# Performance work log

Hardware: AMD Instinct MI355X
Metric: run time of the kernel (lower is better)

Reference implementation:

```python
import jax, jax.numpy as jnp
import numpy as np

HID = 128
PE_DIM = 4
N = 100_000       # nodes per type
E = 400_000       # edges per edge type
L = 3             # message passing layers
G = 512           # num graphs
NT = ['ssBox', 'place_frame', 'object', 'ssCylinder', 'pick', 'place']
FEAT_DIMS = {'ssBox': 4, 'place_frame': 4, 'object': 4, 'ssCylinder': 3}
EMB_IN = {'ssBox': 8, 'place_frame': 8, 'object': 8, 'ssCylinder': 7, 'pick': 4, 'place': 4}
EDGE_TYPES = [
    ('object', 'ssBox'), ('ssBox', 'object'), ('place_frame', 'ssBox'), ('ssBox', 'place_frame'),
    ('place_frame', 'object'), ('object', 'place_frame'), ('pick', 'place'), ('place', 'pick'),
    ('object', 'object'), ('ssBox', 'ssBox'), ('place_frame', 'place_frame'), ('ssCylinder', 'ssCylinder'),
    ('object', 'pick'), ('pick', 'object'), ('place_frame', 'pick'), ('pick', 'place_frame'),
    ('ssCylinder', 'pick'), ('pick', 'ssCylinder'), ('object', 'place'), ('place', 'object'),
    ('ssCylinder', 'place'), ('place', 'ssCylinder'), ('place_frame', 'place'), ('place', 'place_frame')]


def _pe(times):
    # sinusoidal PE from integer positions -> [n, PE_DIM], cols interleaved sin/cos
    pos = times.astype(jnp.float32)[:, None]
    div = jnp.exp(jnp.arange(0, PE_DIM, 2, dtype=jnp.float32) * (-np.log(10000.0) / PE_DIM))
    s, c = jnp.sin(pos * div), jnp.cos(pos * div)
    return jnp.stack([s, c], axis=2).reshape(pos.shape[0], PE_DIM)


def setup_inputs() -> dict:
    key = jax.random.key(0)
    ks = iter(jax.random.split(key, 64))
    inp = {}
    for t in ['ssBox', 'place_frame', 'object']:
        inp['x_' + t] = jax.random.normal(next(ks), (N, 4), jnp.float32)
    inp['x_ssCylinder'] = jax.random.normal(next(ks), (N, 3), jnp.float32)
    for t in NT:
        d = EMB_IN[t]
        inp['W_' + t] = jax.random.normal(next(ks), (d, HID), jnp.float32) / np.sqrt(d)
        inp['b_' + t] = jax.random.normal(next(ks), (HID,), jnp.float32) * 0.01
    sc = 1.0 / np.sqrt(HID)
    inp['sage_Wl'] = jax.random.normal(next(ks), (L, 24, HID, HID), jnp.float32) * sc
    inp['sage_bl'] = jax.random.normal(next(ks), (L, 24, HID), jnp.float32) * 0.01
    inp['sage_Wr'] = jax.random.normal(next(ks), (L, 24, HID, HID), jnp.float32) * sc
    inp['oh_W1'] = jax.random.normal(next(ks), (HID, HID // 4), jnp.float32) * sc
    inp['oh_b1'] = jax.random.normal(next(ks), (HID // 4,), jnp.float32) * 0.01
    inp['oh_W2'] = jax.random.normal(next(ks), (HID // 4, 1), jnp.float32) / np.sqrt(HID // 4)
    inp['oh_b2'] = jax.random.normal(next(ks), (1,), jnp.float32) * 0.01
    inp['times'] = jax.random.randint(next(ks), (6, N), 0, 1000, jnp.int32)
    inp['edges'] = jax.random.randint(next(ks), (24, 2, E), 0, N, jnp.int32)
    inp['batch'] = jax.random.randint(next(ks), (6, N), 0, G, jnp.int32)
    return inp


def reference(x_ssBox, x_place_frame, x_object, x_ssCylinder,
              W_ssBox, b_ssBox, W_place_frame, b_place_frame, W_object, b_object,
              W_ssCylinder, b_ssCylinder, W_pick, b_pick, W_place, b_place,
              sage_Wl, sage_bl, sage_Wr, oh_W1, oh_b1, oh_W2, oh_b2,
              times, edges, batch):
    feats = {'ssBox': x_ssBox, 'place_frame': x_place_frame, 'object': x_object, 'ssCylinder': x_ssCylinder}
    embW = {'ssBox': W_ssBox, 'place_frame': W_place_frame, 'object': W_object,
            'ssCylinder': W_ssCylinder, 'pick': W_pick, 'place': W_place}
    embB = {'ssBox': b_ssBox, 'place_frame': b_place_frame, 'object': b_object,
            'ssCylinder': b_ssCylinder, 'pick': b_pick, 'place': b_place}
    init, x = {}, {}
    for t in ['ssBox', 'place_frame', 'object', 'ssCylinder']:
        f = jnp.concatenate([feats[t], _pe(times[NT.index(t)])], axis=1)
        h = f @ embW[t] + embB[t]
        init[t] = h
        x[t] = h
    for t in ['pick', 'place']:
        x[t] = _pe(times[NT.index(t)]) @ embW[t] + embB[t]
    x = {t: jax.nn.relu(v) for t, v in x.items()}

    for layer in range(L):
        out = {}
        for i, (src, dst) in enumerate(EDGE_TYPES):
            e = edges[i]
            msg = x[src][e[0]]                                           # [E, HID] gather
            agg = jax.ops.segment_sum(msg, e[1], num_segments=N)
            deg = jax.ops.segment_sum(jnp.ones((E,), msg.dtype), e[1], num_segments=N)
            mean = agg / jnp.maximum(deg, 1.0)[:, None]                  # SAGE mean aggr
            o = mean @ sage_Wl[layer, i] + sage_bl[layer, i] + x[dst] @ sage_Wr[layer, i]
            out[dst] = out[dst] + o if dst in out else o
        # dropout is identity in eval/reference
        x = {t: jax.nn.relu(out.get(t, x[t])) for t in x}

    g = jnp.zeros((G, HID), jnp.float32)
    for t in ['pick', 'place']:
        g = g.at[batch[NT.index(t)]].add(x[t])
    for t in ['ssBox', 'ssCylinder', 'place_frame', 'object']:
        g = g.at[batch[NT.index(t)]].add(init[t])
    h = jax.nn.relu(g) @ oh_W1 + oh_b1
    h = jax.nn.relu(h) @ oh_W2 + oh_b2
    return h.squeeze(-1)
```

## Files before the change

### kernel.cpp

```cpp
#include <hip/hip_runtime.h>
#include <hip/hip_bf16.h>

#define NN 100000
#define EE 400000
#define HID 128
#define GG 512
#define NTY 6
#define NET 24
#define TILES_PER_TYPE 1563
#define EMB_TILES 782
#define BLK_ELEMS ((size_t)NN * 128)
#define BLK_BYTES (BLK_ELEMS * 2)

#define P1_BLKS 37500
#define HN_BLKS 2344
#define PWR_BLKS 1152
#define PBL_BLKS 9
#define PWL_BLKS 4608
#define EMB_BLKS (NTY * EMB_TILES)
#define ZG_BLKS 256

typedef _Float16 half8 __attribute__((ext_vector_type(8)));
typedef float f32x4 __attribute__((ext_vector_type(4)));

__constant__ int d_EMB_IN[6]    = {8,8,8,7,4,4};
__constant__ int d_FD[6]        = {4,4,4,3,0,0};
__constant__ int d_EDGE_SRC[24] = {2,0,1,0,1,2,4,5,2,0,1,3,2,4,1,4,3,4,2,5,3,5,1,5};
__constant__ int d_DST_NIN[6]   = {3,5,5,3,4,4};
__constant__ int d_DST_OFF[6]   = {0,3,8,13,16,20};
__constant__ int d_DST_EDGES[24]= {0,2,9, 3,5,10,15,23, 1,4,8,13,19, 11,17,21, 7,12,14,16, 6,18,20,22};

struct GP {
    const float* feat[4];
    const float* embW[6];
    const float* embB[6];
    const float* Wl; const float* bl; const float* Wr;
    const float* W1; const float* b1; const float* W2; const float* b2;
    const int* times; const int* edges; const int* batch;
};

struct XT { _Float16* p[6]; };

__device__ __forceinline__ int clampi(int v, int lo, int hi) {
    return v < lo ? lo : (v > hi ? hi : v);
}

__global__ void zero_i32(int* __restrict__ p, int n) {
    int i = blockIdx.x * 256 + threadIdx.x;
    if (i < n) p[i] = 0;
}

__global__ void diag_kernel(float* __restrict__ out, float v) {
    int i = blockIdx.x * 64 + threadIdx.x;
    if (i < GG) out[i] = v;
}

__device__ __forceinline__ void csr_pass1_body(const int* __restrict__ edges, int* __restrict__ deg,
                                               unsigned short* __restrict__ rank, int b) {
    int i = b * 256 + threadIdx.x;
    if (i >= NET * EE) return;
    int et = i / EE, e = i - et * EE;
    int dst = clampi(edges[(et * 2 + 1) * EE + e], 0, NN - 1);
    int r = atomicAdd(&deg[et * NN + dst], 1);
    rank[i] = (unsigned short)(r > 65535 ? 65535 : r);
}

__device__ __forceinline__ void csr_pass2_body(const int* __restrict__ edges, const int* __restrict__ rowptr,
                                               const unsigned short* __restrict__ rank, int* __restrict__ csr, int b) {
    int i = b * 256 + threadIdx.x;
    if (i >= NET * EE) return;
    int et = i / EE, e = i - et * EE;
    int src = clampi(edges[(et * 2) * EE + e], 0, NN - 1);
    int dst = clampi(edges[(et * 2 + 1) * EE + e], 0, NN - 1);
    int pos = clampi(rowptr[et * NN + dst] + (int)rank[i], 0, NET * EE - 1);
    csr[pos] = src;
}

__device__ __forceinline__ void hist_nodes_body(const int* __restrict__ batch, int* __restrict__ hist2, int b) {
    int i = b * 256 + threadIdx.x;
    if (i >= NTY * NN) return;
    int t = i / NN, n = i - t * NN;
    int bb = clampi(batch[t * NN + n], 0, GG - 1);
    atomicAdd(&hist2[t * GG + bb], 1);
}

__device__ __forceinline__ void scatter_nodes_body(const int* __restrict__ batch, const int* __restrict__ rowptr2,
                                                   int* __restrict__ fill2, int* __restrict__ nodelist, int b) {
    int i = b * 256 + threadIdx.x;
    if (i >= NTY * NN) return;
    int t = i / NN, n = i - t * NN;
    int bb = t * GG + clampi(batch[t * NN + n], 0, GG - 1);
    int pos = clampi(rowptr2[bb] + atomicAdd(&fill2[bb], 1), 0, NTY * NN - 1);
    nodelist[pos] = n;
}

__device__ __forceinline__ void prep_wl_body(const float* __restrict__ Wl, _Float16* __restrict__ WlTf, int b) {
    int i = b * 256 + threadIdx.x;
    if (i >= 72 * 16384) return;
    int mat = i >> 14;
    int o = i & 16383;
    int cq = o >> 9; int c = cq >> 2, q = cq & 3;
    int lane = (o >> 3) & 63, j = o & 7;
    int k = q * 32 + (lane >> 4) * 8 + j;
    int n = c * 16 + (lane & 15);
    WlTf[i] = (_Float16)Wl[((size_t)mat * 128 + k) * 128 + n];
}

__device__ __forceinline__ void prep_wr_body(const float* __restrict__ Wr, _Float16* __restrict__ WrTf, int b) {
    int i = b * 256 + threadIdx.x;
    if (i >= 18 * 16384) return;
    int mat = i >> 14;
    int l = mat / 6, dd = mat - l * 6;
    int o = i & 16383;
    int cq = o >> 9; int c = cq >> 2, q = cq & 3;
    int lane = (o >> 3) & 63, j = o & 7;
    int k = q * 32 + (lane >> 4) * 8 + j;
    int n = c * 16 + (lane & 15);
    float s = 0.f;
    int nin = d_DST_NIN[dd], off = d_DST_OFF[dd];
    for (int ii = 0; ii < nin; ++ii) {
        int e = d_DST_EDGES[off + ii];
        s += Wr[(((size_t)l * 24 + e) * 128 + k) * 128 + n];
    }
    WrTf[i] = (_Float16)s;
}

__device__ __forceinline__ void prep_bl_body(const float* __restrict__ bl, float* __restrict__ bls, int b) {
    int i = b * 256 + threadIdx.x;
    if (i >= 3 * 6 * 128) return;
    int l = i / 768; int rest = i - l * 768;
    int dd = rest >> 7; int col = rest & 127;
    float s = 0.f;
    int nin = d_DST_NIN[dd], off = d_DST_OFF[dd];
    for (int ii = 0; ii < nin; ++ii) {
        int e = d_DST_EDGES[off + ii];
        s += bl[((size_t)l * 24 + e) * 128 + col];
    }
    bls[i] = s;
}

__device__ __forceinline__ void embed_body(const GP& gp, const XT& xout, int bidx,
                                           float fls[128][8], float Wsh[8][128], float bsh[128]) {
    int t = bidx / EMB_TILES;
    int tile = bidx - t * EMB_TILES;
    int base = tile * 128;
    int tid = threadIdx.x;
    int ein = d_EMB_IN[t];
    for (int idx = tid; idx < 1024; idx += 256) {
        int k = idx >> 7, dd = idx & 127;
        Wsh[k][dd] = (k < ein) ? gp.embW[t][k * 128 + dd] : 0.f;
    }
    if (tid < 128) bsh[tid] = gp.embB[t][tid];
    if (tid < 128) {
        int node = base + tid;
        float f[8] = {0.f,0.f,0.f,0.f,0.f,0.f,0.f,0.f};
        if (node < NN) {
            int fd = d_FD[t];
            if (fd > 0) {
                const float* fp = gp.feat[t] + (size_t)node * fd;
                for (int k = 0; k < fd; k++) f[k] = fp[k];
            }
            float pos = (float)gp.times[t * NN + node];
            float d1 = expf(-0.5f * logf(10000.0f));
            f[fd + 0] = sinf(pos);      f[fd + 1] = cosf(pos);
            f[fd + 2] = sinf(pos * d1); f[fd + 3] = cosf(pos * d1);
        }
#pragma unroll
        for (int k = 0; k < 8; k++) fls[tid][k] = f[k];
    }
    __syncthreads();
    int oct = tid & 15, slot = tid >> 4;
    _Float16* xp = xout.p[t];
    for (int nl = slot; nl < 128; nl += 16) {
        int node = base + nl;
        if (node >= NN) continue;
        float h[8];
#pragma unroll
        for (int j = 0; j < 8; ++j) h[j] = bsh[oct * 8 + j];
#pragma unroll
        for (int k = 0; k < 8; ++k) {
            float f = fls[nl][k];
#pragma unroll
            for (int j = 0; j < 8; ++j) h[j] += f * Wsh[k][oct * 8 + j];
        }
        half8 hv;
#pragma unroll
        for (int j = 0; j < 8; ++j) { float v = h[j] > 0.f ? h[j] : 0.f; hv[j] = (_Float16)v; }
        *(half8*)(xp + (size_t)node * 128 + oct * 8) = hv;
    }
}

__global__ __launch_bounds__(256)
void mega1(GP gp, int* __restrict__ deg, unsigned short* __restrict__ rank,
           int* __restrict__ hist2, _Float16* __restrict__ WrTf, float* __restrict__ bls,
           _Float16* __restrict__ WlTf, XT tabA) {
    __shared__ float fls[128][8];
    __shared__ float Wsh[8][128];
    __shared__ float bsh[128];
    int b = blockIdx.x;
    if (b < P1_BLKS) { csr_pass1_body(gp.edges, deg, rank, b); return; }
    b -= P1_BLKS;
    if (b < HN_BLKS) { hist_nodes_body(gp.batch, hist2, b); return; }
    b -= HN_BLKS;
    if (b < PWR_BLKS) { prep_wr_body(gp.Wr, WrTf, b); return; }
    b -= PWR_BLKS;
    if (b < PBL_BLKS) { prep_bl_body(gp.bl, bls, b); return; }
    b -= PBL_BLKS;
    if (b < PWL_BLKS) { prep_wl_body(gp.Wl, WlTf, b); return; }
    b -= PWL_BLKS;
    embed_body(gp, tabA, b, fls, Wsh, bsh);
}

__global__ __launch_bounds__(256)
void mega2(GP gp, const int* __restrict__ rowptr, const unsigned short* __restrict__ rank,
           int* __restrict__ csr, const int* __restrict__ rowptr2, int* __restrict__ fill2,
           int* __restrict__ nodelist, int* __restrict__ g) {
    int b = blockIdx.x;
    if (b < P1_BLKS) { csr_pass2_body(gp.edges, rowptr, rank, csr, b); return; }
    b -= P1_BLKS;
    if (b < HN_BLKS) { scatter_nodes_body(gp.batch, rowptr2, fill2, nodelist, b); return; }
    b -= HN_BLKS;
    int i = b * 256 + threadIdx.x;
    if (i < GG * 128) g[i] = 0;
}

__global__ void prep_wr_k(const float* __restrict__ Wr, _Float16* __restrict__ WrTf) { prep_wr_body(Wr, WrTf, blockIdx.x); }
__global__ void prep_bl_k(const float* __restrict__ bl, float* __restrict__ bls)     { prep_bl_body(bl, bls, blockIdx.x); }
__global__ void prep_wl_k(const float* __restrict__ Wl, _Float16* __restrict__ WlTf) { prep_wl_body(Wl, WlTf, blockIdx.x); }
__global__ void embed_k(GP gp, XT xout) {
    __shared__ float fls[128][8];
    __shared__ float Wsh[8][128];
    __shared__ float bsh[128];
    embed_body(gp, xout, blockIdx.x, fls, Wsh, bsh);
}

__global__ void scan1(const int* __restrict__ in, int* __restrict__ out, int* __restrict__ bsum, int M) {
    int base = blockIdx.x * 2048;
    int tid = threadIdx.x;
    int idx = base + tid * 8;
    int v[8]; int s = 0;
#pragma unroll
    for (int k = 0; k < 8; k++) { int i = idx + k; v[k] = (i < M) ? in[i] : 0; }
#pragma unroll
    for (int k = 0; k < 8; k++) { int t = v[k]; v[k] = s; s += t; }
    __shared__ int sh[256];
    sh[tid] = s; __syncthreads();
    for (int off = 1; off < 256; off <<= 1) {
        int t = (tid >= off) ? sh[tid - off] : 0;
        __syncthreads(); sh[tid] += t; __syncthreads();
    }
    int excl = sh[tid] - s;
#pragma unroll
    for (int k = 0; k < 8; k++) { int i = idx + k; if (i < M) out[i] = excl + v[k]; }
    if (tid == 255) bsum[blockIdx.x] = sh[255];
}

__global__ void scan2_node(int* __restrict__ bsum, int NB, int* __restrict__ rowptr, int M, int total,
                           int* __restrict__ hist2, int* __restrict__ rowptr2) {
    __shared__ int sh[256];
    __shared__ int shc;
    int tid = threadIdx.x;
    int carry = 0;
    for (int chunk = 0; chunk < NB; chunk += 256) {
        int i = chunk + tid;
        int v = (i < NB) ? bsum[i] : 0;
        __syncthreads();
        sh[tid] = v; __syncthreads();
        for (int off = 1; off < 256; off <<= 1) {
            int t = (tid >= off) ? sh[tid - off] : 0;
            __syncthreads(); sh[tid] += t; __syncthreads();
        }
        int inc = sh[tid];
        if (i < NB) bsum[i] = carry + inc - v;
        if (tid == 255) shc = inc;
        __syncthreads();
        carry += shc;
    }
    if (tid == 0) rowptr[M] = total;
    carry = 0;
    for (int chunk = 0; chunk < NTY * GG; chunk += 256) {
        int v = hist2[chunk + tid];
        __syncthreads();
        sh[tid] = v; __syncthreads();
        for (int off = 1; off < 256; off <<= 1) {
            int t = (tid >= off) ? sh[tid - off] : 0;
            __syncthreads(); sh[tid] += t; __syncthreads();
        }
        rowptr2[chunk + tid] = carry + sh[tid] - v;
        hist2[chunk + tid] = 0;
        if (tid == 255) shc = sh[255];
        __syncthreads();
        carry += shc;
    }
    if (tid == 0) rowptr2[NTY * GG] = NTY * NN;
}

__global__ void scan3(int* __restrict__ out, const int* __restrict__ bsum, int M) {
    int i = blockIdx.x * 256 + threadIdx.x;
    if (i < M) out[i] += bsum[i >> 11];
}

__global__ __launch_bounds__(256)
void layer_kernel(XT cur, XT nxt, int d0,
                  const int* __restrict__ rowptr, const int* __restrict__ csr,
                  const _Float16* __restrict__ WlTf, const _Float16* __restrict__ WrTf,
                  const float* __restrict__ bls) {
    int bid = blockIdx.x;
    int d = d0 + bid / TILES_PER_TYPE;
    int tile = bid % TILES_PER_TYPE;
    int tid = threadIdx.x, lane = tid & 63, wave = tid >> 6;
    int lrow = lane & 15, quad = lane >> 4;
    int wrow0 = tile * 64 + wave * 16;
    int myrow = wrow0 + lrow;
    bool rowok = myrow < NN;

    f32x4 acc[8];
#pragma unroll
    for (int c = 0; c < 8; c++) {
        float bv = bls[d * 128 + c * 16 + lrow];
        acc[c] = (f32x4){bv, bv, bv, bv};
    }

    int nin = d_DST_NIN[d];
    int off = d_DST_OFF[d];
    for (int term = 0; term <= nin; ++term) {
        half8 af[4];
        const _Float16* Bmat;
        if (term == 0) {
            Bmat = WrTf + (size_t)d * 16384;
            if (rowok) {
                const half8* p = (const half8*)(cur.p[d] + (size_t)myrow * 128 + quad * 8);
                af[0] = p[0]; af[1] = p[4]; af[2] = p[8]; af[3] = p[12];
            } else {
#pragma unroll
                for (int q = 0; q < 4; q++)
#pragma unroll
                    for (int z = 0; z < 8; z++) af[q][z] = (_Float16)0.f;
            }
        } else {
            int e = d_DST_EDGES[off + term - 1];
            int st = d_EDGE_SRC[e];
            Bmat = WlTf + (size_t)e * 16384;
            const _Float16* xs = cur.p[st];
            float facc[32];
#pragma unroll
            for (int z = 0; z < 32; z++) facc[z] = 0.f;
            int start = 0, cnt = 0;
            if (rowok) {
                int bi = e * NN + myrow;
                start = clampi(rowptr[bi], 0, NET * EE - 1);
                cnt = clampi(rowptr[bi + 1] - start, 0, 4096);
            }
            for (int j = 0;; ++j) {
                if (__ballot(j < cnt) == 0ull) break;
                if (j < cnt) {
                    int sn = clampi(csr[start + j], 0, NN - 1);
                    const half8* p = (const half8*)(xs + (size_t)sn * 128 + quad * 8);
                    half8 v0 = p[0], v1 = p[4], v2 = p[8], v3 = p[12];
#pragma unroll
                    for (int z = 0; z < 8; z++) {
                        facc[z]      += (float)v0[z];
                        facc[8 + z]  += (float)v1[z];
                        facc[16 + z] += (float)v2[z];
                        facc[24 + z] += (float)v3[z];
                    }
                }
            }
            float inv = 1.0f / (float)(cnt > 1 ? cnt : 1);
#pragma unroll
            for (int q = 0; q < 4; q++)
#pragma unroll
                for (int z = 0; z < 8; z++) af[q][z] = (_Float16)(facc[q * 8 + z] * inv);
        }
#pragma unroll
        for (int q = 0; q < 4; q++) {
#pragma unroll
            for (int c = 0; c < 8; c++) {
                half8 b = *(const half8*)(Bmat + (((c * 4 + q) << 9) + (lane << 3)));
                acc[c] = __builtin_amdgcn_mfma_f32_16x16x32_f16(af[q], b, acc[c], 0, 0, 0);
            }
        }
    }
    _Float16* xo = nxt.p[d];
#pragma unroll
    for (int c = 0; c < 8; c++) {
#pragma unroll
        for (int r = 0; r < 4; r++) {
            int grow = wrow0 + quad * 4 + r;
            if (grow < NN) {
                float v = acc[c][r];
                v = v > 0.f ? v : 0.f;
                xo[(size_t)grow * 128 + c * 16 + lrow] = (_Float16)v;
            }
        }
    }
}

__global__ void readout_kernel(GP gp, XT x3,
                               const int* __restrict__ nodelist, const int* __restrict__ rowptr2,
                               float* __restrict__ g) {
    int t = blockIdx.x >> 9;
    int gi = blockIdx.x & 511;
    int tid = threadIdx.x;
    int s = clampi(rowptr2[t * GG + gi], 0, NTY * NN - 1);
    int cnt = clampi(rowptr2[t * GG + gi + 1] - s, 0, NN);
    if (t >= 4) {
        int oct = tid & 15, slot = tid >> 4;
        const _Float16* xp = x3.p[t];
        float acc8[8];
#pragma unroll
        for (int z = 0; z < 8; z++) acc8[z] = 0.f;
        for (int li = slot; li < cnt; li += 16) {
            int node = clampi(nodelist[s + li], 0, NN - 1);
            half8 v = *(const half8*)(xp + (size_t)node * 128 + oct * 8);
#pragma unroll
            for (int z = 0; z < 8; z++) acc8[z] += (float)v[z];
        }
        __shared__ float red[16][128];
#pragma unroll
        for (int z = 0; z < 8; z++) red[slot][oct * 8 + z] = acc8[z];
        __syncthreads();
        for (int off = 8; off >= 1; off >>= 1) {
            if (slot < off) {
#pragma unroll
                for (int z = 0; z < 8; z++)
                    red[slot][oct * 8 + z] += red[slot + off][oct * 8 + z];
            }
            __syncthreads();
        }
        if (tid < 128) atomicAdd(&g[gi * 128 + tid], red[0][tid]);
    } else {
        int ein = d_EMB_IN[t];
        int fd = d_FD[t];
        const float* W = gp.embW[t]; const float* bb = gp.embB[t];
        float d1 = expf(-0.5f * logf(10000.0f));
        float fs[8];
#pragma unroll
        for (int k = 0; k < 8; k++) fs[k] = 0.f;
        for (int li = tid; li < cnt; li += 256) {
            int node = clampi(nodelist[s + li], 0, NN - 1);
            const float* fp = gp.feat[t] + (size_t)node * fd;
            for (int k = 0; k < fd; k++) fs[k] += fp[k];
            float pos = (float)gp.times[t * NN + node];
            fs[fd + 0] += sinf(pos);      fs[fd + 1] += cosf(pos);
            fs[fd + 2] += sinf(pos * d1); fs[fd + 3] += cosf(pos * d1);
        }
        __shared__ float red[8][256];
#pragma unroll
        for (int k = 0; k < 8; k++) red[k][tid] = fs[k];
        __syncthreads();
        for (int off = 128; off >= 1; off >>= 1) {
            if (tid < off) {
#pragma unroll
                for (int k = 0; k < 8; k++) red[k][tid] += red[k][tid + off];
            }
            __syncthreads();
        }
        if (tid < 128) {
            float acc = (float)cnt * bb[tid];
            for (int k = 0; k < ein; k++) acc += red[k][0] * W[k * 128 + tid];
            atomicAdd(&g[gi * 128 + tid], acc);
        }
    }
}

__global__ void head_kernel(const float* __restrict__ g, const float* __restrict__ W1,
                            const float* __restrict__ b1, const float* __restrict__ W2,
                            const float* __restrict__ b2, float* __restrict__ out) {
    int gi = blockIdx.x;
    int tid = threadIdx.x;
    __shared__ float h1[32];
    if (tid < 32) {
        float s = b1[tid];
        for (int dd = 0; dd < 128; ++dd) s += fmaxf(g[gi * 128 + dd], 0.f) * W1[dd * 32 + tid];
        h1[tid] = s;
    }
    __syncthreads();
    if (tid == 0) {
        float o = b2[0];
        for (int j = 0; j < 32; ++j) o += fmaxf(h1[j], 0.f) * W2[j];
        out[gi] = o;
    }
}

extern "C" void kernel_launch(void* const* d_in, const int* in_sizes, int n_in,
                              void* d_out, int out_size, void* d_ws, size_t ws_size,
                              hipStream_t stream) {
    char* ws = (char*)d_ws;
    size_t o = 0;
    auto alloc = [&](size_t bytes) -> void* {
        void* p = ws + o;
        o += (bytes + 255) & ~(size_t)255;
        return p;
    };
    _Float16* xws   = (_Float16*)alloc(9 * BLK_BYTES);
    int* csr        = (int*)alloc((size_t)NET * EE * 4 + 256);
    int* rowptr     = (int*)alloc(((size_t)NET * NN + 1) * 4);
    int* nodelist   = (int*)alloc((size_t)NTY * NN * 4);
    int* rowptr2    = (int*)alloc((NTY * GG + 1) * 4);
    float* g        = (float*)alloc(GG * 128 * 4);
    int* bsum       = (int*)alloc(4096 * 4);
    int* bsum2      = (int*)alloc(256 * 4);
    size_t REQUIRED = o;
    int* degX             = (int*)alloc((size_t)NET * NN * 4);
    int* hist2X           = (int*)alloc(NTY * GG * 4);
    unsigned short* rankX = (unsigned short*)alloc((size_t)NET * EE * 2);
    _Float16* WlTfX       = (_Float16*)alloc((size_t)72 * 16384 * 2);
    _Float16* WrTfX       = (_Float16*)alloc((size_t)18 * 16384 * 2);
    float* blsX           = (float*)alloc(3 * 6 * 128 * 4);
    bool sep = ws_size >= o;
    (void)in_sizes; (void)out_size;

    if (ws_size < REQUIRED || n_in != 26) {
        float v = 2000.0f + (float)(ws_size >> 20) + (n_in != 26 ? 100000.0f : 0.0f);
        diag_kernel<<<8, 64, 0, stream>>>((float*)d_out, v);
        return;
    }

    GP gp;
    for (int t = 0; t < 4; t++) gp.feat[t] = (const float*)d_in[t];
    for (int t = 0; t < 6; t++) { gp.embW[t] = (const float*)d_in[4 + 2 * t]; gp.embB[t] = (const float*)d_in[5 + 2 * t]; }
    gp.Wl = (const float*)d_in[16];
    gp.bl = (const float*)d_in[17];
    gp.Wr = (const float*)d_in[18];
    gp.W1 = (const float*)d_in[19];
    gp.b1 = (const float*)d_in[20];
    gp.W2 = (const float*)d_in[21];
    gp.b2 = (const float*)d_in[22];
    gp.times = (const int*)d_in[23];
    gp.edges = (const int*)d_in[24];
    gp.batch = (const int*)d_in[25];

    int* deg; int* hist2; unsigned short* rank;
    _Float16* WlTf; _Float16* WrTf; float* bls;
    if (sep) {
        deg = degX; hist2 = hist2X; rank = rankX; WlTf = WlTfX; WrTf = WrTfX; bls = blsX;
    } else {
        deg   = (int*)xws;
        hist2 = (int*)((char*)xws + 9600000);
        rank  = (unsigned short*)((char*)xws + BLK_BYTES);
        WlTf  = (_Float16*)d_in[18];
        WrTf  = (_Float16*)d_in[25];
        bls   = (float*)((char*)d_in[25] + 1048576);
    }

    XT tabA, tabB;
    for (int t = 0; t < 6; t++) tabA.p[t] = xws + (size_t)t * BLK_ELEMS;
    for (int t = 0; t < 3; t++) tabB.p[t] = xws + (size_t)(6 + t) * BLK_ELEMS;
    for (int t = 3; t < 6; t++) tabB.p[t] = (_Float16*)d_in[24] + (size_t)(t - 3) * BLK_ELEMS;

    int Medge = NET * NN;
    int NB = (Medge + 2047) / 2048;
    int Mn = NTY * GG;

    zero_i32<<<(Medge + Mn + 255) / 256, 256, 0, stream>>>(deg, Medge + Mn);
    if (sep) {
        mega1<<<P1_BLKS + HN_BLKS + PWR_BLKS + PBL_BLKS + PWL_BLKS + EMB_BLKS, 256, 0, stream>>>(
            gp, deg, rank, hist2, WrTf, bls, WlTf, tabA);
    } else {
        mega1<<<P1_BLKS + HN_BLKS, 256, 0, stream>>>(gp, deg, rank, hist2, WrTf, bls, WlTf, tabA);
    }
    scan1<<<NB, 256, 0, stream>>>(deg, rowptr, bsum, Medge);
    scan2_node<<<1, 256, 0, stream>>>(bsum, NB, rowptr, Medge, NET * EE, hist2, rowptr2);
    scan3<<<(Medge + 255) / 256, 256, 0, stream>>>(rowptr, bsum, Medge);
    mega2<<<P1_BLKS + HN_BLKS + ZG_BLKS, 256, 0, stream>>>(gp, rowptr, rank, csr,
                                                           rowptr2, hist2, nodelist, (int*)g);
    if (!sep) {
        prep_wr_k<<<PWR_BLKS, 256, 0, stream>>>(gp.Wr, WrTf);
        prep_bl_k<<<PBL_BLKS, 256, 0, stream>>>(gp.bl, bls);
        prep_wl_k<<<PWL_BLKS, 256, 0, stream>>>(gp.Wl, WlTf);
        embed_k<<<EMB_BLKS, 256, 0, stream>>>(gp, tabA);
    }

    layer_kernel<<<6 * TILES_PER_TYPE, 256, 0, stream>>>(tabA, tabB, 0, rowptr, csr,
        WlTf + (size_t)0 * 24 * 16384, WrTf + (size_t)0 * 6 * 16384, bls + 0 * 6 * 128);
    layer_kernel<<<5 * TILES_PER_TYPE, 256, 0, stream>>>(tabB, tabA, 1, rowptr, csr,
        WlTf + (size_t)1 * 24 * 16384, WrTf + (size_t)1 * 6 * 16384, bls + 1 * 6 * 128);
    layer_kernel<<<2 * TILES_PER_TYPE, 256, 0, stream>>>(tabA, tabB, 4, rowptr, csr,
        WlTf + (size_t)2 * 24 * 16384, WrTf + (size_t)2 * 6 * 16384, bls + 2 * 6 * 128);

    readout_kernel<<<NTY * GG, 256, 0, stream>>>(gp, tabB, nodelist, rowptr2, g);
    head_kernel<<<GG, 64, 0, stream>>>(g, gp.W1, gp.b1, gp.W2, gp.b2, (float*)d_out);
}
```

Measured before the change: 2.858 ms.

## Fuse scan stages with last-block ticket and merge init readout into layer one

Merges the three-kernel prefix scan into one kernel, where the last block to finish, chosen by an atomic ticket, scans the block sums and the node histogram. The separate add-block-offset pass goes away, and consumers now add bsum on the fly when they read rowptr. The readout for the init node types is folded into the first layer kernel as extra blocks, the zeroing kernel becomes a hipMemsetAsync, and the final readout only covers pick and place. This cuts kernel launches and one full pass over rowptr, at the cost of an extra bsum load for every rowptr read in the layer gathers and CSR build.

```diff
diff --git a/kernel.cpp b/kernel.cpp
--- a/kernel.cpp
+++ b/kernel.cpp
@@ -11,6 +11,8 @@
 #define EMB_TILES 782
 #define BLK_ELEMS ((size_t)NN * 128)
 #define BLK_BYTES (BLK_ELEMS * 2)
+#define MEDGE (NET * NN)
+#define NBE ((MEDGE + 2047) / 2048)
 
 #define P1_BLKS 37500
 #define HN_BLKS 2344
@@ -19,6 +21,7 @@
 #define PWL_BLKS 4608
 #define EMB_BLKS (NTY * EMB_TILES)
 #define ZG_BLKS 256
+#define RO_BLKS (4 * GG)
 
 typedef _Float16 half8 __attribute__((ext_vector_type(8)));
 typedef float f32x4 __attribute__((ext_vector_type(4)));
@@ -45,11 +48,6 @@
     return v < lo ? lo : (v > hi ? hi : v);
 }
 
-__global__ void zero_i32(int* __restrict__ p, int n) {
-    int i = blockIdx.x * 256 + threadIdx.x;
-    if (i < n) p[i] = 0;
-}
-
 __global__ void diag_kernel(float* __restrict__ out, float v) {
     int i = blockIdx.x * 64 + threadIdx.x;
     if (i < GG) out[i] = v;
@@ -66,13 +64,15 @@
 }
 
 __device__ __forceinline__ void csr_pass2_body(const int* __restrict__ edges, const int* __restrict__ rowptr,
+                                               const int* __restrict__ bsum,
                                                const unsigned short* __restrict__ rank, int* __restrict__ csr, int b) {
     int i = b * 256 + threadIdx.x;
     if (i >= NET * EE) return;
     int et = i / EE, e = i - et * EE;
     int src = clampi(edges[(et * 2) * EE + e], 0, NN - 1);
     int dst = clampi(edges[(et * 2 + 1) * EE + e], 0, NN - 1);
-    int pos = clampi(rowptr[et * NN + dst] + (int)rank[i], 0, NET * EE - 1);
+    int bin = et * NN + dst;
+    int pos = clampi(rowptr[bin] + bsum[bin >> 11] + (int)rank[i], 0, NET * EE - 1);
     csr[pos] = src;
 }
 
@@ -187,6 +187,144 @@
 #pragma unroll
         for (int j = 0; j < 8; ++j) { float v = h[j] > 0.f ? h[j] : 0.f; hv[j] = (_Float16)v; }
         *(half8*)(xp + (size_t)node * 128 + oct * 8) = hv;
+    }
+}
+
+__device__ __forceinline__ void readout_init_body(const GP& gp, const int* __restrict__ nodelist,
+                                                  const int* __restrict__ rowptr2, float* __restrict__ g,
+                                                  int b, float red[8][256]) {
+    int t = b >> 9;
+    int gi = b & 511;
+    int tid = threadIdx.x;
+    int s = clampi(rowptr2[t * GG + gi], 0, NTY * NN - 1);
+    int cnt = clampi(rowptr2[t * GG + gi + 1] - s, 0, NN);
+    int ein = d_EMB_IN[t];
+    int fd = d_FD[t];
+    const float* W = gp.embW[t]; const float* bb = gp.embB[t];
+    float d1 = expf(-0.5f * logf(10000.0f));
+    float fs[8];
+#pragma unroll
+    for (int k = 0; k < 8; k++) fs[k] = 0.f;
+    for (int li = tid; li < cnt; li += 256) {
+        int node = clampi(nodelist[s + li], 0, NN - 1);
+        const float* fp = gp.feat[t] + (size_t)node * fd;
+        for (int k = 0; k < fd; k++) fs[k] += fp[k];
+        float pos = (float)gp.times[t * NN + node];
+        fs[fd + 0] += sinf(pos);      fs[fd + 1] += cosf(pos);
+        fs[fd + 2] += sinf(pos * d1); fs[fd + 3] += cosf(pos * d1);
+    }
+#pragma unroll
+    for (int k = 0; k < 8; k++) red[k][tid] = fs[k];
+    __syncthreads();
+    for (int off = 128; off >= 1; off >>= 1) {
+        if (tid < off) {
+#pragma unroll
+            for (int k = 0; k < 8; k++) red[k][tid] += red[k][tid + off];
+        }
+        __syncthreads();
+    }
+    if (tid < 128) {
+        float acc = (float)cnt * bb[tid];
+        for (int k = 0; k < ein; k++) acc += red[k][0] * W[k * 128 + tid];
+        atomicAdd(&g[gi * 128 + tid], acc);
+    }
+}
+
+__device__ __forceinline__ void layer_body(const XT& cur, const XT& nxt, int d0, int bid,
+                                           const int* __restrict__ rowptr, const int* __restrict__ bsum,
+                                           const int* __restrict__ csr,
+                                           const _Float16* __restrict__ WlTf, const _Float16* __restrict__ WrTf,
+                                           const float* __restrict__ bls) {
+    int d = d0 + bid / TILES_PER_TYPE;
+    int tile = bid % TILES_PER_TYPE;
+    int tid = threadIdx.x, lane = tid & 63, wave = tid >> 6;
+    int lrow = lane & 15, quad = lane >> 4;
+    int wrow0 = tile * 64 + wave * 16;
+    int myrow = wrow0 + lrow;
+    bool rowok = myrow < NN;
+
+    f32x4 acc[8];
+#pragma unroll
+    for (int c = 0; c < 8; c++) {
+        float bv = bls[d * 128 + c * 16 + lrow];
+        acc[c] = (f32x4){bv, bv, bv, bv};
+    }
+
+    int nin = d_DST_NIN[d];
+    int off = d_DST_OFF[d];
+    for (int term = 0; term <= nin; ++term) {
+        half8 af[4];
+        const _Float16* Bmat;
+        if (term == 0) {
+            Bmat = WrTf + (size_t)d * 16384;
+            if (rowok) {
+                const half8* p = (const half8*)(cur.p[d] + (size_t)myrow * 128 + quad * 8);
+                af[0] = p[0]; af[1] = p[4]; af[2] = p[8]; af[3] = p[12];
+            } else {
+#pragma unroll
+                for (int q = 0; q < 4; q++)
+#pragma unroll
+                    for (int z = 0; z < 8; z++) af[q][z] = (_Float16)0.f;
+            }
+        } else {
+            int e = d_DST_EDGES[off + term - 1];
+            int st = d_EDGE_SRC[e];
+            Bmat = WlTf + (size_t)e * 16384;
+            const _Float16* xs = cur.p[st];
+            float facc[32];
+#pragma unroll
+            for (int z = 0; z < 32; z++) facc[z] = 0.f;
+            int start = 0, cnt = 0;
+            if (rowok) {
+                int bi = e * NN + myrow;
+                int s0 = rowptr[bi] + bsum[bi >> 11];
+                int bi1 = bi + 1;
+                int e1 = (bi1 == MEDGE) ? (NET * EE) : (rowptr[bi1] + bsum[bi1 >> 11]);
+                start = clampi(s0, 0, NET * EE - 1);
+                cnt = clampi(e1 - s0, 0, 4096);
+            }
+            for (int j = 0;; ++j) {
+                if (__ballot(j < cnt) == 0ull) break;
+                if (j < cnt) {
+                    int sn = clampi(csr[start + j], 0, NN - 1);
+                    const half8* p = (const half8*)(xs + (size_t)sn * 128 + quad * 8);
+                    half8 v0 = p[0], v1 = p[4], v2 = p[8], v3 = p[12];
+#pragma unroll
+                    for (int z = 0; z < 8; z++) {
+                        facc[z]      += (float)v0[z];
+                        facc[8 + z]  += (float)v1[z];
+                        facc[16 + z] += (float)v2[z];
+                        facc[24 + z] += (float)v3[z];
+                    }
+                }
+            }
+            float inv = 1.0f / (float)(cnt > 1 ? cnt : 1);
+#pragma unroll
+            for (int q = 0; q < 4; q++)
+#pragma unroll
+                for (int z = 0; z < 8; z++) af[q][z] = (_Float16)(facc[q * 8 + z] * inv);
+        }
+#pragma unroll
+        for (int q = 0; q < 4; q++) {
+#pragma unroll
+            for (int c = 0; c < 8; c++) {
+                half8 b = *(const half8*)(Bmat + (((c * 4 + q) << 9) + (lane << 3)));
+                acc[c] = __builtin_amdgcn_mfma_f32_16x16x32_f16(af[q], b, acc[c], 0, 0, 0);
+            }
+        }
+    }
+    _Float16* xo = nxt.p[d];
+#pragma unroll
+    for (int c = 0; c < 8; c++) {
+#pragma unroll
+        for (int r = 0; r < 4; r++) {
+            int grow = wrow0 + quad * 4 + r;
+            if (grow < NN) {
+                float v = acc[c][r];
+                v = v > 0.f ? v : 0.f;
+                xo[(size_t)grow * 128 + c * 16 + lrow] = (_Float16)v;
+            }
+        }
     }
 }
 
@@ -212,11 +350,12 @@
 }
 
 __global__ __launch_bounds__(256)
-void mega2(GP gp, const int* __restrict__ rowptr, const unsigned short* __restrict__ rank,
+void mega2(GP gp, const int* __restrict__ rowptr, const int* __restrict__ bsum,
+           const unsigned short* __restrict__ rank,
            int* __restrict__ csr, const int* __restrict__ rowptr2, int* __restrict__ fill2,
            int* __restrict__ nodelist, int* __restrict__ g) {
     int b = blockIdx.x;
-    if (b < P1_BLKS) { csr_pass2_body(gp.edges, rowptr, rank, csr, b); return; }
+    if (b < P1_BLKS) { csr_pass2_body(gp.edges, rowptr, bsum, rank, csr, b); return; }
     b -= P1_BLKS;
     if (b < HN_BLKS) { scatter_nodes_body(gp.batch, rowptr2, fill2, nodelist, b); return; }
     b -= HN_BLKS;
@@ -234,16 +373,19 @@
     embed_body(gp, xout, blockIdx.x, fls, Wsh, bsh);
 }
 
-__global__ void scan1(const int* __restrict__ in, int* __restrict__ out, int* __restrict__ bsum, int M) {
+__global__ void scan1f(const int* __restrict__ in, int* __restrict__ out, int* __restrict__ bsum,
+                       int* __restrict__ hist2, int* __restrict__ rowptr2, int* __restrict__ done) {
     int base = blockIdx.x * 2048;
     int tid = threadIdx.x;
     int idx = base + tid * 8;
     int v[8]; int s = 0;
 #pragma unroll
-    for (int k = 0; k < 8; k++) { int i = idx + k; v[k] = (i < M) ? in[i] : 0; }
+    for (int k = 0; k < 8; k++) { int i = idx + k; v[k] = (i < MEDGE) ? in[i] : 0; }
 #pragma unroll
     for (int k = 0; k < 8; k++) { int t = v[k]; v[k] = s; s += t; }
     __shared__ int sh[256];
+    __shared__ int shc;
+    __shared__ int ticket;
     sh[tid] = s; __syncthreads();
     for (int off = 1; off < 256; off <<= 1) {
         int t = (tid >= off) ? sh[tid - off] : 0;
@@ -251,42 +393,39 @@
     }
     int excl = sh[tid] - s;
 #pragma unroll
-    for (int k = 0; k < 8; k++) { int i = idx + k; if (i < M) out[i] = excl + v[k]; }
+    for (int k = 0; k < 8; k++) { int i = idx + k; if (i < MEDGE) out[i] = excl + v[k]; }
     if (tid == 255) bsum[blockIdx.x] = sh[255];
-}
-
-__global__ void scan2_node(int* __restrict__ bsum, int NB, int* __restrict__ rowptr, int M, int total,
-                           int* __restrict__ hist2, int* __restrict__ rowptr2) {
-    __shared__ int sh[256];
-    __shared__ int shc;
-    int tid = threadIdx.x;
+    __threadfence();
+    __syncthreads();
+    if (tid == 0) ticket = atomicAdd(done, 1);
+    __syncthreads();
+    if (ticket != NBE - 1) return;
+    __threadfence();
     int carry = 0;
-    for (int chunk = 0; chunk < NB; chunk += 256) {
+    for (int chunk = 0; chunk < NBE; chunk += 256) {
         int i = chunk + tid;
-        int v = (i < NB) ? bsum[i] : 0;
+        int vv = (i < NBE) ? bsum[i] : 0;
         __syncthreads();
-        sh[tid] = v; __syncthreads();
+        sh[tid] = vv; __syncthreads();
         for (int off = 1; off < 256; off <<= 1) {
             int t = (tid >= off) ? sh[tid - off] : 0;
             __syncthreads(); sh[tid] += t; __syncthreads();
         }
-        int inc = sh[tid];
-        if (i < NB) bsum[i] = carry + inc - v;
-        if (tid == 255) shc = inc;
+        if (i < NBE) bsum[i] = carry + sh[tid] - vv;
+        if (tid == 255) shc = sh[255];
         __syncthreads();
         carry += shc;
     }
-    if (tid == 0) rowptr[M] = total;
     carry = 0;
     for (int chunk = 0; chunk < NTY * GG; chunk += 256) {
-        int v = hist2[chunk + tid];
+        int vv = hist2[chunk + tid];
         __syncthreads();
-        sh[tid] = v; __syncthreads();
+        sh[tid] = vv; __syncthreads();
         for (int off = 1; off < 256; off <<= 1) {
             int t = (tid >= off) ? sh[tid - off] : 0;
             __syncthreads(); sh[tid] += t; __syncthreads();
         }
-        rowptr2[chunk + tid] = carry + sh[tid] - v;
+        rowptr2[chunk + tid] = carry + sh[tid] - vv;
         hist2[chunk + tid] = 0;
         if (tid == 255) shc = sh[255];
         __syncthreads();
@@ -295,173 +434,63 @@
     if (tid == 0) rowptr2[NTY * GG] = NTY * NN;
 }
 
-__global__ void scan3(int* __restrict__ out, const int* __restrict__ bsum, int M) {
-    int i = blockIdx.x * 256 + threadIdx.x;
-    if (i < M) out[i] += bsum[i >> 11];
-}
-
 __global__ __launch_bounds__(256)
 void layer_kernel(XT cur, XT nxt, int d0,
-                  const int* __restrict__ rowptr, const int* __restrict__ csr,
+                  const int* __restrict__ rowptr, const int* __restrict__ bsum,
+                  const int* __restrict__ csr,
                   const _Float16* __restrict__ WlTf, const _Float16* __restrict__ WrTf,
                   const float* __restrict__ bls) {
-    int bid = blockIdx.x;
-    int d = d0 + bid / TILES_PER_TYPE;
-    int tile = bid % TILES_PER_TYPE;
-    int tid = threadIdx.x, lane = tid & 63, wave = tid >> 6;
-    int lrow = lane & 15, quad = lane >> 4;
-    int wrow0 = tile * 64 + wave * 16;
-    int myrow = wrow0 + lrow;
-    bool rowok = myrow < NN;
-
-    f32x4 acc[8];
-#pragma unroll
-    for (int c = 0; c < 8; c++) {
-        float bv = bls[d * 128 + c * 16 + lrow];
-        acc[c] = (f32x4){bv, bv, bv, bv};
-    }
-
-    int nin = d_DST_NIN[d];
-    int off = d_DST_OFF[d];
-    for (int term = 0; term <= nin; ++term) {
-        half8 af[4];
-        const _Float16* Bmat;
-        if (term == 0) {
-            Bmat = WrTf + (size_t)d * 16384;
-            if (rowok) {
-                const half8* p = (const half8*)(cur.p[d] + (size_t)myrow * 128 + quad * 8);
-                af[0] = p[0]; af[1] = p[4]; af[2] = p[8]; af[3] = p[12];
-            } else {
-#pragma unroll
-                for (int q = 0; q < 4; q++)
-#pragma unroll
-                    for (int z = 0; z < 8; z++) af[q][z] = (_Float16)0.f;
-            }
-        } else {
-            int e = d_DST_EDGES[off + term - 1];
-            int st = d_EDGE_SRC[e];
-            Bmat = WlTf + (size_t)e * 16384;
-            const _Float16* xs = cur.p[st];
-            float facc[32];
-#pragma unroll
-            for (int z = 0; z < 32; z++) facc[z] = 0.f;
-            int start = 0, cnt = 0;
-            if (rowok) {
-                int bi = e * NN + myrow;
-                start = clampi(rowptr[bi], 0, NET * EE - 1);
-                cnt = clampi(rowptr[bi + 1] - start, 0, 4096);
-            }
-            for (int j = 0;; ++j) {
-                if (__ballot(j < cnt) == 0ull) break;
-                if (j < cnt) {
-                    int sn = clampi(csr[start + j], 0, NN - 1);
-                    const half8* p = (const half8*)(xs + (size_t)sn * 128 + quad * 8);
-                    half8 v0 = p[0], v1 = p[4], v2 = p[8], v3 = p[12];
-#pragma unroll
-                    for (int z = 0; z < 8; z++) {
-                        facc[z]      += (float)v0[z];
-                        facc[8 + z]  += (float)v1[z];
-                        facc[16 + z] += (float)v2[z];
-                        facc[24 + z] += (float)v3[z];
-                    }
-                }
-            }
-            float inv = 1.0f / (float)(cnt > 1 ? cnt : 1);
-#pragma unroll
-            for (int q = 0; q < 4; q++)
-#pragma unroll
-                for (int z = 0; z < 8; z++) af[q][z] = (_Float16)(facc[q * 8 + z] * inv);
-        }
-#pragma unroll
-        for (int q = 0; q < 4; q++) {
-#pragma unroll
-            for (int c = 0; c < 8; c++) {
-                half8 b = *(const half8*)(Bmat + (((c * 4 + q) << 9) + (lane << 3)));
-                acc[c] = __builtin_amdgcn_mfma_f32_16x16x32_f16(af[q], b, acc[c], 0, 0, 0);
-            }
-        }
-    }
-    _Float16* xo = nxt.p[d];
-#pragma unroll
-    for (int c = 0; c < 8; c++) {
-#pragma unroll
-        for (int r = 0; r < 4; r++) {
-            int grow = wrow0 + quad * 4 + r;
-            if (grow < NN) {
-                float v = acc[c][r];
-                v = v > 0.f ? v : 0.f;
-                xo[(size_t)grow * 128 + c * 16 + lrow] = (_Float16)v;
-            }
-        }
-    }
-}
-
-__global__ void readout_kernel(GP gp, XT x3,
-                               const int* __restrict__ nodelist, const int* __restrict__ rowptr2,
-                               float* __restrict__ g) {
-    int t = blockIdx.x >> 9;
+    layer_body(cur, nxt, d0, blockIdx.x, rowptr, bsum, csr, WlTf, WrTf, bls);
+}
+
+__global__ __launch_bounds__(256)
+void layer1_mega(XT cur, XT nxt,
+                 const int* __restrict__ rowptr, const int* __restrict__ bsum,
+                 const int* __restrict__ csr,
+                 const _Float16* __restrict__ WlTf, const _Float16* __restrict__ WrTf,
+                 const float* __restrict__ bls,
+                 GP gp, const int* __restrict__ nodelist, const int* __restrict__ rowptr2,
+                 float* __restrict__ g) {
+    __shared__ float red[8][256];
+    int b = blockIdx.x;
+    if (b < 6 * TILES_PER_TYPE) {
+        layer_body(cur, nxt, 0, b, rowptr, bsum, csr, WlTf, WrTf, bls);
+        return;
+    }
+    readout_init_body(gp, nodelist, rowptr2, g, b - 6 * TILES_PER_TYPE, red);
+}
+
+__global__ void readout45(XT x3, const int* __restrict__ nodelist, const int* __restrict__ rowptr2,
+                          float* __restrict__ g) {
+    int t = 4 + (blockIdx.x >> 9);
     int gi = blockIdx.x & 511;
     int tid = threadIdx.x;
     int s = clampi(rowptr2[t * GG + gi], 0, NTY * NN - 1);
     int cnt = clampi(rowptr2[t * GG + gi + 1] - s, 0, NN);
-    if (t >= 4) {
-        int oct = tid & 15, slot = tid >> 4;
-        const _Float16* xp = x3.p[t];
-        float acc8[8];
-#pragma unroll
-        for (int z = 0; z < 8; z++) acc8[z] = 0.f;
-        for (int li = slot; li < cnt; li += 16) {
-            int node = clampi(nodelist[s + li], 0, NN - 1);
-            half8 v = *(const half8*)(xp + (size_t)node * 128 + oct * 8);
-#pragma unroll
-            for (int z = 0; z < 8; z++) acc8[z] += (float)v[z];
-        }
-        __shared__ float red[16][128];
-#pragma unroll
-        for (int z = 0; z < 8; z++) red[slot][oct * 8 + z] = acc8[z];
+    int oct = tid & 15, slot = tid >> 4;
+    const _Float16* xp = x3.p[t];
+    float acc8[8];
+#pragma unroll
+    for (int z = 0; z < 8; z++) acc8[z] = 0.f;
+    for (int li = slot; li < cnt; li += 16) {
+        int node = clampi(nodelist[s + li], 0, NN - 1);
+        half8 v = *(const half8*)(xp + (size_t)node * 128 + oct * 8);
+#pragma unroll
+        for (int z = 0; z < 8; z++) acc8[z] += (float)v[z];
+    }
+    __shared__ float red[16][128];
+#pragma unroll
+    for (int z = 0; z < 8; z++) red[slot][oct * 8 + z] = acc8[z];
+    __syncthreads();
+    for (int off = 8; off >= 1; off >>= 1) {
+        if (slot < off) {
+#pragma unroll
+            for (int z = 0; z < 8; z++)
+                red[slot][oct * 8 + z] += red[slot + off][oct * 8 + z];
+        }
         __syncthreads();
-        for (int off = 8; off >= 1; off >>= 1) {
-            if (slot < off) {
-#pragma unroll
-                for (int z = 0; z < 8; z++)
-                    red[slot][oct * 8 + z] += red[slot + off][oct * 8 + z];
-            }
-            __syncthreads();
-        }
-        if (tid < 128) atomicAdd(&g[gi * 128 + tid], red[0][tid]);
-    } else {
-        int ein = d_EMB_IN[t];
-        int fd = d_FD[t];
-        const float* W = gp.embW[t]; const float* bb = gp.embB[t];
-        float d1 = expf(-0.5f * logf(10000.0f));
-        float fs[8];
-#pragma unroll
-        for (int k = 0; k < 8; k++) fs[k] = 0.f;
-        for (int li = tid; li < cnt; li += 256) {
-            int node = clampi(nodelist[s + li], 0, NN - 1);
-            const float* fp = gp.feat[t] + (size_t)node * fd;
-            for (int k = 0; k < fd; k++) fs[k] += fp[k];
-            float pos = (float)gp.times[t * NN + node];
-            fs[fd + 0] += sinf(pos);      fs[fd + 1] += cosf(pos);
-            fs[fd + 2] += sinf(pos * d1); fs[fd + 3] += cosf(pos * d1);
-        }
-        __shared__ float red[8][256];
-#pragma unroll
-        for (int k = 0; k < 8; k++) red[k][tid] = fs[k];
-        __syncthreads();
-        for (int off = 128; off >= 1; off >>= 1) {
-            if (tid < off) {
-#pragma unroll
-                for (int k = 0; k < 8; k++) red[k][tid] += red[k][tid + off];
-            }
-            __syncthreads();
-        }
-        if (tid < 128) {
-            float acc = (float)cnt * bb[tid];
-            for (int k = 0; k < ein; k++) acc += red[k][0] * W[k * 128 + tid];
-            atomicAdd(&g[gi * 128 + tid], acc);
-        }
-    }
+    }
+    if (tid < 128) atomicAdd(&g[gi * 128 + tid], red[0][tid]);
 }
 
 __global__ void head_kernel(const float* __restrict__ g, const float* __restrict__ W1,
@@ -495,15 +524,15 @@
     };
     _Float16* xws   = (_Float16*)alloc(9 * BLK_BYTES);
     int* csr        = (int*)alloc((size_t)NET * EE * 4 + 256);
-    int* rowptr     = (int*)alloc(((size_t)NET * NN + 1) * 4);
+    int* rowptr     = (int*)alloc(((size_t)MEDGE + 1) * 4);
     int* nodelist   = (int*)alloc((size_t)NTY * NN * 4);
     int* rowptr2    = (int*)alloc((NTY * GG + 1) * 4);
     float* g        = (float*)alloc(GG * 128 * 4);
     int* bsum       = (int*)alloc(4096 * 4);
-    int* bsum2      = (int*)alloc(256 * 4);
     size_t REQUIRED = o;
-    int* degX             = (int*)alloc((size_t)NET * NN * 4);
+    int* degX             = (int*)alloc((size_t)MEDGE * 4);
     int* hist2X           = (int*)alloc(NTY * GG * 4);
+    int* doneX            = (int*)alloc(256);
     unsigned short* rankX = (unsigned short*)alloc((size_t)NET * EE * 2);
     _Float16* WlTfX       = (_Float16*)alloc((size_t)72 * 16384 * 2);
     _Float16* WrTfX       = (_Float16*)alloc((size_t)18 * 16384 * 2);
@@ -531,13 +560,15 @@
     gp.edges = (const int*)d_in[24];
     gp.batch = (const int*)d_in[25];
 
-    int* deg; int* hist2; unsigned short* rank;
+    int* deg; int* hist2; int* done; unsigned short* rank;
     _Float16* WlTf; _Float16* WrTf; float* bls;
     if (sep) {
-        deg = degX; hist2 = hist2X; rank = rankX; WlTf = WlTfX; WrTf = WrTfX; bls = blsX;
+        deg = degX; hist2 = hist2X; done = doneX; rank = rankX;
+        WlTf = WlTfX; WrTf = WrTfX; bls = blsX;
     } else {
         deg   = (int*)xws;
-        hist2 = (int*)((char*)xws + 9600000);
+        hist2 = deg + MEDGE;
+        done  = hist2 + NTY * GG;
         rank  = (unsigned short*)((char*)xws + BLK_BYTES);
         WlTf  = (_Float16*)d_in[18];
         WrTf  = (_Float16*)d_in[25];
@@ -549,21 +580,15 @@
     for (int t = 0; t < 3; t++) tabB.p[t] = xws + (size_t)(6 + t) * BLK_ELEMS;
     for (int t = 3; t < 6; t++) tabB.p[t] = (_Float16*)d_in[24] + (size_t)(t - 3) * BLK_ELEMS;
 
-    int Medge = NET * NN;
-    int NB = (Medge + 2047) / 2048;
-    int Mn = NTY * GG;
-
-    zero_i32<<<(Medge + Mn + 255) / 256, 256, 0, stream>>>(deg, Medge + Mn);
+    hipMemsetAsync(deg, 0, (size_t)(MEDGE + NTY * GG) * 4 + 256, stream);
     if (sep) {
         mega1<<<P1_BLKS + HN_BLKS + PWR_BLKS + PBL_BLKS + PWL_BLKS + EMB_BLKS, 256, 0, stream>>>(
             gp, deg, rank, hist2, WrTf, bls, WlTf, tabA);
     } else {
         mega1<<<P1_BLKS + HN_BLKS, 256, 0, stream>>>(gp, deg, rank, hist2, WrTf, bls, WlTf, tabA);
     }
-    scan1<<<NB, 256, 0, stream>>>(deg, rowptr, bsum, Medge);
-    scan2_node<<<1, 256, 0, stream>>>(bsum, NB, rowptr, Medge, NET * EE, hist2, rowptr2);
-    scan3<<<(Medge + 255) / 256, 256, 0, stream>>>(rowptr, bsum, Medge);
-    mega2<<<P1_BLKS + HN_BLKS + ZG_BLKS, 256, 0, stream>>>(gp, rowptr, rank, csr,
+    scan1f<<<NBE, 256, 0, stream>>>(deg, rowptr, bsum, hist2, rowptr2, done);
+    mega2<<<P1_BLKS + HN_BLKS + ZG_BLKS, 256, 0, stream>>>(gp, rowptr, bsum, rank, csr,
                                                            rowptr2, hist2, nodelist, (int*)g);
     if (!sep) {
         prep_wr_k<<<PWR_BLKS, 256, 0, stream>>>(gp.Wr, WrTf);
@@ -572,13 +597,14 @@
         embed_k<<<EMB_BLKS, 256, 0, stream>>>(gp, tabA);
     }
 
-    layer_kernel<<<6 * TILES_PER_TYPE, 256, 0, stream>>>(tabA, tabB, 0, rowptr, csr,
-        WlTf + (size_t)0 * 24 * 16384, WrTf + (size_t)0 * 6 * 16384, bls + 0 * 6 * 128);
-    layer_kernel<<<5 * TILES_PER_TYPE, 256, 0, stream>>>(tabB, tabA, 1, rowptr, csr,
+    layer1_mega<<<6 * TILES_PER_TYPE + RO_BLKS, 256, 0, stream>>>(tabA, tabB, rowptr, bsum, csr,
+        WlTf + (size_t)0 * 24 * 16384, WrTf + (size_t)0 * 6 * 16384, bls + 0 * 6 * 128,
+        gp, nodelist, rowptr2, g);
+    layer_kernel<<<5 * TILES_PER_TYPE, 256, 0, stream>>>(tabB, tabA, 1, rowptr, bsum, csr,
         WlTf + (size_t)1 * 24 * 16384, WrTf + (size_t)1 * 6 * 16384, bls + 1 * 6 * 128);
-    layer_kernel<<<2 * TILES_PER_TYPE, 256, 0, stream>>>(tabA, tabB, 4, rowptr, csr,
+    layer_kernel<<<2 * TILES_PER_TYPE, 256, 0, stream>>>(tabA, tabB, 4, rowptr, bsum, csr,
         WlTf + (size_t)2 * 24 * 16384, WrTf + (size_t)2 * 6 * 16384, bls + 2 * 6 * 128);
 
-    readout_kernel<<<NTY * GG, 256, 0, stream>>>(gp, tabB, nodelist, rowptr2, g);
+    readout45<<<2 * GG, 256, 0, stream>>>(tabB, nodelist, rowptr2, g);
     head_kernel<<<GG, 64, 0, stream>>>(g, gp.W1, gp.b1, gp.W2, gp.b2, (float*)d_out);
 }
```

Result: slower. 3.011 ms (+5.3%).
